# Kernel tuning notes

Hardware: AMD Instinct MI355X
Metric: run time of the kernel (lower is better)

The kernel has to match this reference:

```python
import jax, jax.numpy as jnp
import numpy as np

S, N, F = 32, 512, 256        # systems, atoms per system, feature/charge channels
R_EXCL = 5.0                  # neighbor_list_options.cutoff -> exclusion_radius
BOX = 30.0                    # box edge for random positions (Angstrom-scale)


def setup_inputs() -> dict:
    key = jax.random.key(0)
    k1, k2, k3, k4 = jax.random.split(key, 4)
    positions = jax.random.uniform(k1, (S, N, 3), dtype=jnp.float32) * BOX
    features = jax.random.normal(k2, (S * N, F), dtype=jnp.float32)
    W = jax.random.normal(k3, (F, F), dtype=jnp.float32) / jnp.sqrt(F)
    b = jax.random.normal(k4, (F,), dtype=jnp.float32) * 0.01
    return {"positions": positions, "features": features, "W": W, "b": b}


def _pair_potential(d):
    # CoulombPotential(smearing=None, exclusion_radius=R_EXCL).from_dist:
    # v(r) = (1/r) * (1 - f_cut(r)),  f_cut = 0.5*(1 + cos(pi*r/R_EXCL)) for r < R_EXCL
    fcut = jnp.where(d < R_EXCL, 0.5 * (1.0 + jnp.cos(jnp.pi * d / R_EXCL)), 0.0)
    return (1.0 / d) * (1.0 - fcut)


def reference(positions, features, W, b):
    # charges_map: Linear(F, F)
    charges = features @ W.T + b                      # [S*N, F]
    q = charges.reshape(S, N, F)                      # per-system charges

    # all-pairs distances per system (torch.combinations path, both directions
    # accumulated by the half-neighbor-list Calculator)
    diff = positions[:, :, None, :] - positions[:, None, :, :]   # [S,N,N,3]
    d = jnp.sqrt(jnp.sum(diff * diff, axis=-1))                  # [S,N,N]
    eye = jnp.eye(N, dtype=bool)
    d_safe = jnp.where(eye, 1.0, d)
    v = jnp.where(eye, 0.0, _pair_potential(d_safe))             # [S,N,N]

    # V_i = 0.5 * sum_j v(r_ij) q_j  (torchpme energy convention E = sum_i q_i V_i)
    V = 0.5 * jnp.einsum('sij,sjf->sif', v, q)                   # [S,N,F]

    # module returns potential * charges, concatenated over systems
    return (V * q).reshape(S * N, F)
```

## Files before the change

kernel.cpp:

```cpp
#include <hip/hip_runtime.h>
#include <hip/hip_cooperative_groups.h>

#define SY 32
#define NA 512
#define FD 256

typedef __attribute__((ext_vector_type(8))) short bf16x8;
typedef __attribute__((ext_vector_type(4))) short bf16x4;
typedef __attribute__((ext_vector_type(4))) float f32x4;

static __device__ __forceinline__ short f2bf(float x) {
    union { float f; unsigned u; } v; v.f = x;
    unsigned r = v.u + 0x7fffu + ((v.u >> 16) & 1u);
    return (short)(r >> 16);
}
static __device__ __forceinline__ float bf2f(short x) {
    union { float f; unsigned u; } v;
    v.u = ((unsigned)(unsigned short)x) << 16;
    return v.f;
}

__global__ __launch_bounds__(512) void charges_mfma(
    const float* __restrict__ feat, const float* __restrict__ W,
    const float* __restrict__ b, float* __restrict__ qfp,
    short* __restrict__ qT)
{
    __shared__ __attribute__((aligned(16))) short sA[64 * 72];
    __shared__ __attribute__((aligned(16))) short sB[256 * 72];
    __shared__ __attribute__((aligned(16))) short tr[256 * 72];
    const int t    = threadIdx.x;
    const int i0   = blockIdx.x * 64;
    const int w    = t >> 6;
    const int lane = t & 63;
    const int n16  = lane & 15;
    const int quad = lane >> 4;

    f32x4 acc[4][2];
    #pragma unroll
    for (int a = 0; a < 4; ++a)
        #pragma unroll
        for (int c = 0; c < 2; ++c) acc[a][c] = (f32x4)0.0f;

    for (int k0 = 0; k0 < FD; k0 += 64) {
        #pragma unroll
        for (int m = 0; m < 2; ++m) {
            int lin = t + 512 * m;
            int i = lin >> 4, kq = lin & 15;
            float4 v = *(const float4*)&feat[(size_t)(i0 + i) * FD + k0 + 4 * kq];
            bf16x4 p; p[0] = f2bf(v.x); p[1] = f2bf(v.y);
                      p[2] = f2bf(v.z); p[3] = f2bf(v.w);
            *(bf16x4*)&sA[i * 72 + 4 * kq] = p;
        }
        #pragma unroll
        for (int m = 0; m < 8; ++m) {
            int lin = t + 512 * m;
            int f = lin >> 4, kq = lin & 15;
            float4 v = *(const float4*)&W[(size_t)f * FD + k0 + 4 * kq];
            bf16x4 p; p[0] = f2bf(v.x); p[1] = f2bf(v.y);
                      p[2] = f2bf(v.z); p[3] = f2bf(v.w);
            *(bf16x4*)&sB[f * 72 + 4 * kq] = p;
        }
        __syncthreads();

        #pragma unroll
        for (int ks = 0; ks < 64; ks += 32) {
            bf16x8 af[4], bfr[2];
            #pragma unroll
            for (int it = 0; it < 4; ++it)
                af[it] = *(const bf16x8*)&sA[(16 * it + n16) * 72 + ks + quad * 8];
            #pragma unroll
            for (int fb = 0; fb < 2; ++fb)
                bfr[fb] = *(const bf16x8*)&sB[(32 * w + 16 * fb + n16) * 72 + ks + quad * 8];
            #pragma unroll
            for (int it = 0; it < 4; ++it)
                #pragma unroll
                for (int fb = 0; fb < 2; ++fb)
                    acc[it][fb] = __builtin_amdgcn_mfma_f32_16x16x32_bf16(
                        af[it], bfr[fb], acc[it][fb], 0, 0, 0);
        }
        __syncthreads();
    }

    float bias[2];
    #pragma unroll
    for (int fb = 0; fb < 2; ++fb) bias[fb] = b[32 * w + 16 * fb + n16];

    if (qfp) {
        #pragma unroll
        for (int it = 0; it < 4; ++it)
            #pragma unroll
            for (int fb = 0; fb < 2; ++fb)
                #pragma unroll
                for (int r = 0; r < 4; ++r) {
                    int i = i0 + 16 * it + 4 * quad + r;
                    int f = 32 * w + 16 * fb + n16;
                    qfp[(size_t)i * FD + f] = acc[it][fb][r] + bias[fb];
                }
    }

    #pragma unroll
    for (int it = 0; it < 4; ++it)
        #pragma unroll
        for (int fb = 0; fb < 2; ++fb) {
            bf16x4 p;
            #pragma unroll
            for (int r = 0; r < 4; ++r) p[r] = f2bf(acc[it][fb][r] + bias[fb]);
            int f = 32 * w + 16 * fb + n16;
            *(bf16x4*)&tr[f * 72 + 16 * it + 4 * quad] = p;
        }
    __syncthreads();
    {
        short* qTs = qT + ((size_t)(i0 >> 9)) * FD * NA;
        const int ilb = i0 & 511;
        #pragma unroll
        for (int n = 0; n < 4; ++n) {
            int S = n * 512 + t;
            int f = S >> 3;
            int c = S & 7;
            uint4 v = *(const uint4*)&tr[f * 72 + c * 8];
            *(uint4*)&qTs[(size_t)f * NA + ilb + c * 8] = v;
        }
    }
}

__global__ __launch_bounds__(256) void lr_fast(
    const float* __restrict__ pos, float* __restrict__ gbuf,
    const short* __restrict__ qT)
{
    __shared__ float px[NA], py[NA], pz[NA];
    __shared__ __attribute__((aligned(16))) short sqb[FD * 64];
    __shared__ __attribute__((aligned(16))) short svb[32 * 64];

    const int blk = blockIdx.x;
    const int s   = blk & 31;
    const int i0  = (blk >> 5) * 32;
    const int t   = threadIdx.x;
    const int w    = t >> 6;
    const int lane = t & 63;
    const int n16  = lane & 15;
    const int quad = lane >> 4;

    for (int m = t; m < NA; m += 256) {
        const float* p = &pos[((size_t)s * NA + m) * 3];
        px[m] = p[0]; py[m] = p[1]; pz[m] = p[2];
    }

    f32x4 acc[2][4];
    #pragma unroll
    for (int a = 0; a < 2; ++a)
        #pragma unroll
        for (int c = 0; c < 4; ++c) acc[a][c] = (f32x4)0.0f;
    float qreg[2][4][4];

    const short* qTs = qT + (size_t)s * FD * NA;
    const int pi = t & 31;
    const int pc = t >> 5;
    const int gi = i0 + pi;

    __syncthreads();
    const float xi = px[gi], yi = py[gi], zi = pz[gi];

    for (int j0 = 0; j0 < NA; j0 += 64) {
        #pragma unroll
        for (int n = 0; n < 8; ++n) {
            int S  = n * 256 + t;
            int f  = S >> 3;
            int cs = S & 7;
            int c  = (cs - f) & 7;
            uint4 v = *(const uint4*)&qTs[(size_t)f * NA + j0 + c * 8];
            *(uint4*)&sqb[f * 64 + cs * 8] = v;
        }
        bf16x8 vrow;
        #pragma unroll
        for (int jj = 0; jj < 8; ++jj) {
            int gj = j0 + pc * 8 + jj;
            float dx = xi - px[gj];
            float dy = yi - py[gj];
            float dz = zi - pz[gj];
            float r2 = dx * dx + dy * dy + dz * dz;
            float inv = __builtin_amdgcn_rsqf(r2);
            float dd  = r2 * inv;
            float sn = __sinf(dd * 0.31415926535f);
            float om = (dd < 5.0f) ? sn * sn : 1.0f;
            float vv = (gi != gj) ? 0.5f * om * inv : 0.0f;
            vrow[jj] = f2bf(vv);
        }
        *(bf16x8*)&svb[pi * 64 + (((pc + pi) & 7) * 8)] = vrow;
        __syncthreads();

        if (j0 == (i0 & ~63)) {
            const int jb0 = i0 & 63;
            #pragma unroll
            for (int it = 0; it < 2; ++it)
                #pragma unroll
                for (int fb = 0; fb < 4; ++fb) {
                    int f = 64 * w + 16 * fb + n16;
                    #pragma unroll
                    for (int r = 0; r < 4; ++r) {
                        int jl = jb0 + 16 * it + 4 * quad + r;
                        int c  = jl >> 3, o = jl & 7;
                        qreg[it][fb][r] =
                            bf2f(sqb[f * 64 + (((c + f) & 7) * 8) + o]);
                    }
                }
        }

        bf16x8 af[2][2], bfr[2][4];
        #pragma unroll
        for (int it = 0; it < 2; ++it)
            #pragma unroll
            for (int kh = 0; kh < 2; ++kh) {
                int i = 16 * it + n16;
                int c = kh * 4 + quad;
                af[it][kh] = *(const bf16x8*)&svb[i * 64 + (((c + i) & 7) * 8)];
            }
        #pragma unroll
        for (int fb = 0; fb < 4; ++fb)
            #pragma unroll
            for (int kh = 0; kh < 2; ++kh) {
                int f = 64 * w + 16 * fb + n16;
                int c = kh * 4 + quad;
                bfr[kh][fb] = *(const bf16x8*)&sqb[f * 64 + (((c + f) & 7) * 8)];
            }
        #pragma unroll
        for (int kh = 0; kh < 2; ++kh)
            #pragma unroll
            for (int it = 0; it < 2; ++it)
                #pragma unroll
                for (int fb = 0; fb < 4; ++fb)
                    acc[it][fb] = __builtin_amdgcn_mfma_f32_16x16x32_bf16(
                        af[it][kh], bfr[kh][fb], acc[it][fb], 0, 0, 0);
        __syncthreads();
    }

    #pragma unroll
    for (int it = 0; it < 2; ++it)
        #pragma unroll
        for (int fb = 0; fb < 4; ++fb)
            #pragma unroll
            for (int r = 0; r < 4; ++r) {
                int i = i0 + 16 * it + 4 * quad + r;
                int f = 64 * w + 16 * fb + n16;
                size_t a = ((size_t)s * NA + i) * FD + f;
                gbuf[a] = acc[it][fb][r] * qreg[it][fb][r];
            }
}

__global__ __launch_bounds__(256) void lr_coop(
    const float* __restrict__ pos, float* __restrict__ gbuf)
{
    __shared__ float px[NA], py[NA], pz[NA];
    __shared__ __attribute__((aligned(16))) short svb[64 * 40];
    __shared__ __attribute__((aligned(16))) short sqb[FD * 40];

    const int blk = blockIdx.x;
    const int s   = blk & 31;
    const int i0  = (blk >> 5) * 64;
    const int t   = threadIdx.x;
    const int w    = t >> 6;
    const int lane = t & 63;
    const int n16  = lane & 15;
    const int quad = lane >> 4;

    for (int m = t; m < NA; m += 256) {
        const float* p = &pos[((size_t)s * NA + m) * 3];
        px[m] = p[0]; py[m] = p[1]; pz[m] = p[2];
    }

    f32x4 acc[4][4];
    #pragma unroll
    for (int a = 0; a < 4; ++a)
        #pragma unroll
        for (int c = 0; c < 4; ++c) acc[a][c] = (f32x4)0.0f;

    __syncthreads();

    const int fq  = t >> 2;
    const int jb  = t & 3;
    const int iv  = t & 63;
    const int jbv = t >> 6;
    const int gi  = i0 + iv;

    float4 rq[8];
    #pragma unroll
    for (int m = 0; m < 8; ++m)
        rq[m] = *(const float4*)&gbuf[((size_t)s * NA + 8 * jb + m) * FD + 4 * fq];

    for (int j0 = 0; j0 < NA; j0 += 32) {
        bf16x8 vrow;
        #pragma unroll
        for (int jj = 0; jj < 8; ++jj) {
            int gj = j0 + 8 * jbv + jj;
            float dx = px[gi] - px[gj];
            float dy = py[gi] - py[gj];
            float dz = pz[gi] - pz[gj];
            float dd = sqrtf(dx * dx + dy * dy + dz * dz);
            float om = (dd < 5.0f) ? 0.5f * (1.0f - __cosf(dd * 0.62831853071795f))
                                   : 1.0f;
            float vv = (gi != gj) ? (0.5f * om * __builtin_amdgcn_rcpf(dd)) : 0.0f;
            vrow[jj] = f2bf(vv);
        }
        bf16x8 rows[4];
        #pragma unroll
        for (int m = 0; m < 8; ++m) {
            rows[0][m] = f2bf(rq[m].x);
            rows[1][m] = f2bf(rq[m].y);
            rows[2][m] = f2bf(rq[m].z);
            rows[3][m] = f2bf(rq[m].w);
        }
        #pragma unroll
        for (int d = 0; d < 4; ++d) {
            int f = 4 * fq + d;
            int phys = (jb + (f >> 3)) & 3;
            *(bf16x8*)&sqb[f * 40 + phys * 8] = rows[d];
        }
        {
            int phys = (jbv + (iv >> 3)) & 3;
            *(bf16x8*)&svb[iv * 40 + phys * 8] = vrow;
        }
        {
            int jn = (j0 + 32) & (NA - 1);
            #pragma unroll
            for (int m = 0; m < 8; ++m)
                rq[m] = *(const float4*)&gbuf[((size_t)s * NA + jn + 8 * jb + m) * FD + 4 * fq];
        }
        __syncthreads();

        bf16x8 af[4], bfr[4];
        #pragma unroll
        for (int it = 0; it < 4; ++it) {
            int i = 16 * it + n16;
            int phys = (quad + (i >> 3)) & 3;
            af[it] = *(const bf16x8*)&svb[i * 40 + phys * 8];
        }
        #pragma unroll
        for (int fb = 0; fb < 4; ++fb) {
            int f = 16 * (4 * w + fb) + n16;
            int phys = (quad + (f >> 3)) & 3;
            bfr[fb] = *(const bf16x8*)&sqb[f * 40 + phys * 8];
        }
        #pragma unroll
        for (int it = 0; it < 4; ++it)
            #pragma unroll
            for (int fb = 0; fb < 4; ++fb)
                acc[it][fb] = __builtin_amdgcn_mfma_f32_16x16x32_bf16(
                    af[it], bfr[fb], acc[it][fb], 0, 0, 0);
        __syncthreads();
    }

    cooperative_groups::this_grid().sync();

    #pragma unroll
    for (int it = 0; it < 4; ++it)
        #pragma unroll
        for (int fb = 0; fb < 4; ++fb)
            #pragma unroll
            for (int r = 0; r < 4; ++r) {
                int i = i0 + 16 * it + 4 * quad + r;
                int f = 16 * (4 * w + fb) + n16;
                size_t a = ((size_t)s * NA + i) * FD + f;
                gbuf[a] = acc[it][fb][r] * gbuf[a];
            }
}

extern "C" void kernel_launch(void* const* d_in, const int* in_sizes, int n_in,
                              void* d_out, int out_size, void* d_ws, size_t ws_size,
                              hipStream_t stream) {
    const float* positions = (const float*)d_in[0];
    const float* features  = (const float*)d_in[1];
    const float* W         = (const float*)d_in[2];
    const float* b         = (const float*)d_in[3];
    float* gbuf = (float*)d_out;

    const size_t qT_bytes = (size_t)SY * NA * FD * sizeof(short);
    const bool fast = (ws_size >= qT_bytes);
    short* qT = fast ? (short*)d_ws : nullptr;

    if (fast) {
        charges_mfma<<<dim3(256), 512, 0, stream>>>(features, W, b, nullptr, qT);
        lr_fast<<<dim3(512), 256, 0, stream>>>(positions, gbuf, qT);
    } else {
        charges_mfma<<<dim3(256), 512, 0, stream>>>(features, W, b, gbuf,
                                                    (short*)d_out );
        void* args[] = {(void*)&positions, (void*)&gbuf};
        hipLaunchCooperativeKernel((void*)lr_coop, dim3(256), dim3(256),
                                   args, 0, stream);
    }
}
```

Baseline: 110.2 us.

## Pre-convert W to bf16, retile charges GEMM, split lr_fast over features with prefetch

A new prep_w kernel converts W to bf16 once per call, so the charges GEMM loads bf16 W directly instead of converting the whole W in every block. The charges kernel now uses 32-row tiles on 256 threads, giving 512 blocks, and reuses sB as the transpose buffer. lr_fast splits the feature dimension into two halves, giving 1024 blocks with a smaller LDS footprint and launch_bounds(256,4) to raise occupancy. It also register-prefetches the next q tile while computing the pair potential. The costs are an extra launch, recomputing the pair potentials twice per system tile, and higher register pressure from the prefetch.

After: 125.8 us. 1.14x slower.

```diff
diff --git a/kernel.cpp b/kernel.cpp
--- a/kernel.cpp
+++ b/kernel.cpp
@@ -20,120 +20,141 @@
     return v.f;
 }
 
-__global__ __launch_bounds__(512) void charges_mfma(
-    const float* __restrict__ feat, const float* __restrict__ W,
-    const float* __restrict__ b, float* __restrict__ qfp,
-    short* __restrict__ qT)
+__global__ __launch_bounds__(256) void prep_w(
+    const float* __restrict__ W, short* __restrict__ Wb)
 {
-    __shared__ __attribute__((aligned(16))) short sA[64 * 72];
+    int idx = (blockIdx.x * 256 + threadIdx.x) * 4;
+    float4 v = *(const float4*)&W[idx];
+    bf16x4 p; p[0] = f2bf(v.x); p[1] = f2bf(v.y);
+              p[2] = f2bf(v.z); p[3] = f2bf(v.w);
+    *(bf16x4*)&Wb[idx] = p;
+}
+
+__global__ __launch_bounds__(256) void charges_v3(
+    const float* __restrict__ feat, const float* __restrict__ Wfp,
+    const short* __restrict__ Wb, const float* __restrict__ b,
+    float* __restrict__ qfp, short* __restrict__ qT)
+{
+    __shared__ __attribute__((aligned(16))) short sA[32 * 72];
     __shared__ __attribute__((aligned(16))) short sB[256 * 72];
-    __shared__ __attribute__((aligned(16))) short tr[256 * 72];
     const int t    = threadIdx.x;
-    const int i0   = blockIdx.x * 64;
+    const int i0   = blockIdx.x * 32;
     const int w    = t >> 6;
     const int lane = t & 63;
     const int n16  = lane & 15;
     const int quad = lane >> 4;
 
-    f32x4 acc[4][2];
-    #pragma unroll
-    for (int a = 0; a < 4; ++a)
-        #pragma unroll
-        for (int c = 0; c < 2; ++c) acc[a][c] = (f32x4)0.0f;
+    f32x4 acc[2][4];
+    #pragma unroll
+    for (int a = 0; a < 2; ++a)
+        #pragma unroll
+        for (int c = 0; c < 4; ++c) acc[a][c] = (f32x4)0.0f;
 
     for (int k0 = 0; k0 < FD; k0 += 64) {
         #pragma unroll
         for (int m = 0; m < 2; ++m) {
-            int lin = t + 512 * m;
-            int i = lin >> 4, kq = lin & 15;
-            float4 v = *(const float4*)&feat[(size_t)(i0 + i) * FD + k0 + 4 * kq];
+            int lin = t + 256 * m;
+            int row = lin >> 4, kq = lin & 15;
+            float4 v = *(const float4*)&feat[(size_t)(i0 + row) * FD + k0 + 4 * kq];
             bf16x4 p; p[0] = f2bf(v.x); p[1] = f2bf(v.y);
                       p[2] = f2bf(v.z); p[3] = f2bf(v.w);
-            *(bf16x4*)&sA[i * 72 + 4 * kq] = p;
-        }
-        #pragma unroll
-        for (int m = 0; m < 8; ++m) {
-            int lin = t + 512 * m;
-            int f = lin >> 4, kq = lin & 15;
-            float4 v = *(const float4*)&W[(size_t)f * FD + k0 + 4 * kq];
-            bf16x4 p; p[0] = f2bf(v.x); p[1] = f2bf(v.y);
-                      p[2] = f2bf(v.z); p[3] = f2bf(v.w);
-            *(bf16x4*)&sB[f * 72 + 4 * kq] = p;
+            *(bf16x4*)&sA[row * 72 + 4 * kq] = p;
+        }
+        if (Wb) {
+            #pragma unroll
+            for (int n = 0; n < 8; ++n) {
+                int S = t + 256 * n;
+                int f = S >> 3, c = S & 7;
+                uint4 v = *(const uint4*)&Wb[(size_t)f * FD + k0 + c * 8];
+                *(uint4*)&sB[f * 72 + c * 8] = v;
+            }
+        } else {
+            #pragma unroll
+            for (int m = 0; m < 16; ++m) {
+                int lin = t + 256 * m;
+                int f = lin >> 4, kq = lin & 15;
+                float4 v = *(const float4*)&Wfp[(size_t)f * FD + k0 + 4 * kq];
+                bf16x4 p; p[0] = f2bf(v.x); p[1] = f2bf(v.y);
+                          p[2] = f2bf(v.z); p[3] = f2bf(v.w);
+                *(bf16x4*)&sB[f * 72 + 4 * kq] = p;
+            }
         }
         __syncthreads();
 
         #pragma unroll
         for (int ks = 0; ks < 64; ks += 32) {
-            bf16x8 af[4], bfr[2];
-            #pragma unroll
-            for (int it = 0; it < 4; ++it)
+            bf16x8 af[2], bfr[4];
+            #pragma unroll
+            for (int it = 0; it < 2; ++it)
                 af[it] = *(const bf16x8*)&sA[(16 * it + n16) * 72 + ks + quad * 8];
             #pragma unroll
-            for (int fb = 0; fb < 2; ++fb)
-                bfr[fb] = *(const bf16x8*)&sB[(32 * w + 16 * fb + n16) * 72 + ks + quad * 8];
-            #pragma unroll
-            for (int it = 0; it < 4; ++it)
+            for (int fb = 0; fb < 4; ++fb)
+                bfr[fb] = *(const bf16x8*)&sB[(64 * w + 16 * fb + n16) * 72 + ks + quad * 8];
+            #pragma unroll
+            for (int it = 0; it < 2; ++it)
                 #pragma unroll
-                for (int fb = 0; fb < 2; ++fb)
+                for (int fb = 0; fb < 4; ++fb)
                     acc[it][fb] = __builtin_amdgcn_mfma_f32_16x16x32_bf16(
                         af[it], bfr[fb], acc[it][fb], 0, 0, 0);
         }
         __syncthreads();
     }
 
-    float bias[2];
-    #pragma unroll
-    for (int fb = 0; fb < 2; ++fb) bias[fb] = b[32 * w + 16 * fb + n16];
+    float bias[4];
+    #pragma unroll
+    for (int fb = 0; fb < 4; ++fb) bias[fb] = b[64 * w + 16 * fb + n16];
 
     if (qfp) {
         #pragma unroll
-        for (int it = 0; it < 4; ++it)
-            #pragma unroll
-            for (int fb = 0; fb < 2; ++fb)
+        for (int it = 0; it < 2; ++it)
+            #pragma unroll
+            for (int fb = 0; fb < 4; ++fb)
                 #pragma unroll
                 for (int r = 0; r < 4; ++r) {
                     int i = i0 + 16 * it + 4 * quad + r;
-                    int f = 32 * w + 16 * fb + n16;
+                    int f = 64 * w + 16 * fb + n16;
                     qfp[(size_t)i * FD + f] = acc[it][fb][r] + bias[fb];
                 }
     }
 
-    #pragma unroll
-    for (int it = 0; it < 4; ++it)
-        #pragma unroll
-        for (int fb = 0; fb < 2; ++fb) {
-            bf16x4 p;
-            #pragma unroll
-            for (int r = 0; r < 4; ++r) p[r] = f2bf(acc[it][fb][r] + bias[fb]);
-            int f = 32 * w + 16 * fb + n16;
-            *(bf16x4*)&tr[f * 72 + 16 * it + 4 * quad] = p;
-        }
-    __syncthreads();
-    {
+    if (qT) {
+        short* tr = sB;
+        #pragma unroll
+        for (int it = 0; it < 2; ++it)
+            #pragma unroll
+            for (int fb = 0; fb < 4; ++fb) {
+                bf16x4 p;
+                #pragma unroll
+                for (int r = 0; r < 4; ++r) p[r] = f2bf(acc[it][fb][r] + bias[fb]);
+                int f = 64 * w + 16 * fb + n16;
+                *(bf16x4*)&tr[f * 40 + 16 * it + 4 * quad] = p;
+            }
+        __syncthreads();
         short* qTs = qT + ((size_t)(i0 >> 9)) * FD * NA;
         const int ilb = i0 & 511;
         #pragma unroll
         for (int n = 0; n < 4; ++n) {
-            int S = n * 512 + t;
-            int f = S >> 3;
-            int c = S & 7;
-            uint4 v = *(const uint4*)&tr[f * 72 + c * 8];
+            int S = t + 256 * n;
+            int f = S >> 2, c = S & 3;
+            uint4 v = *(const uint4*)&tr[f * 40 + c * 8];
             *(uint4*)&qTs[(size_t)f * NA + ilb + c * 8] = v;
         }
     }
 }
 
-__global__ __launch_bounds__(256) void lr_fast(
-    const float* __restrict__ pos, float* __restrict__ gbuf,
+__global__ __launch_bounds__(256, 4) void lr_fast(
+    const float* __restrict__ pos, float* __restrict__ out,
     const short* __restrict__ qT)
 {
     __shared__ float px[NA], py[NA], pz[NA];
-    __shared__ __attribute__((aligned(16))) short sqb[FD * 64];
+    __shared__ __attribute__((aligned(16))) short sqb[128 * 64];
     __shared__ __attribute__((aligned(16))) short svb[32 * 64];
 
     const int blk = blockIdx.x;
     const int s   = blk & 31;
-    const int i0  = (blk >> 5) * 32;
+    const int rr  = blk >> 5;
+    const int i0  = (rr & 15) * 32;
+    const int f0  = (rr >> 4) * 128;
     const int t   = threadIdx.x;
     const int w    = t >> 6;
     const int lane = t & 63;
@@ -145,30 +166,39 @@
         px[m] = p[0]; py[m] = p[1]; pz[m] = p[2];
     }
 
-    f32x4 acc[2][4];
+    f32x4 acc[2][2];
     #pragma unroll
     for (int a = 0; a < 2; ++a)
         #pragma unroll
-        for (int c = 0; c < 4; ++c) acc[a][c] = (f32x4)0.0f;
-    float qreg[2][4][4];
-
-    const short* qTs = qT + (size_t)s * FD * NA;
+        for (int c = 0; c < 2; ++c) acc[a][c] = (f32x4)0.0f;
+    float qreg[2][2][4];
+
+    const short* qTs = qT + (size_t)s * FD * NA + (size_t)f0 * NA;
     const int pi = t & 31;
     const int pc = t >> 5;
     const int gi = i0 + pi;
 
+    const int sfl[1] = {};  (void)sfl;
+    uint4 pf[4];
+    #pragma unroll
+    for (int n = 0; n < 4; ++n) {
+        int S  = t + 256 * n;
+        int fl = S >> 3;
+        int cs = S & 7;
+        int c  = (cs - fl) & 7;
+        pf[n] = *(const uint4*)&qTs[(size_t)fl * NA + 0 + c * 8];
+    }
+
     __syncthreads();
     const float xi = px[gi], yi = py[gi], zi = pz[gi];
 
     for (int j0 = 0; j0 < NA; j0 += 64) {
         #pragma unroll
-        for (int n = 0; n < 8; ++n) {
-            int S  = n * 256 + t;
-            int f  = S >> 3;
+        for (int n = 0; n < 4; ++n) {
+            int S  = t + 256 * n;
+            int fl = S >> 3;
             int cs = S & 7;
-            int c  = (cs - f) & 7;
-            uint4 v = *(const uint4*)&qTs[(size_t)f * NA + j0 + c * 8];
-            *(uint4*)&sqb[f * 64 + cs * 8] = v;
+            *(uint4*)&sqb[fl * 64 + cs * 8] = pf[n];
         }
         bf16x8 vrow;
         #pragma unroll
@@ -186,6 +216,17 @@
             vrow[jj] = f2bf(vv);
         }
         *(bf16x8*)&svb[pi * 64 + (((pc + pi) & 7) * 8)] = vrow;
+        {
+            int jn = (j0 + 64) & (NA - 1);
+            #pragma unroll
+            for (int n = 0; n < 4; ++n) {
+                int S  = t + 256 * n;
+                int fl = S >> 3;
+                int cs = S & 7;
+                int c  = (cs - fl) & 7;
+                pf[n] = *(const uint4*)&qTs[(size_t)fl * NA + jn + c * 8];
+            }
+        }
         __syncthreads();
 
         if (j0 == (i0 & ~63)) {
@@ -193,19 +234,19 @@
             #pragma unroll
             for (int it = 0; it < 2; ++it)
                 #pragma unroll
-                for (int fb = 0; fb < 4; ++fb) {
-                    int f = 64 * w + 16 * fb + n16;
+                for (int fb = 0; fb < 2; ++fb) {
+                    int fl = 32 * w + 16 * fb + n16;
                     #pragma unroll
                     for (int r = 0; r < 4; ++r) {
                         int jl = jb0 + 16 * it + 4 * quad + r;
                         int c  = jl >> 3, o = jl & 7;
                         qreg[it][fb][r] =
-                            bf2f(sqb[f * 64 + (((c + f) & 7) * 8) + o]);
+                            bf2f(sqb[fl * 64 + (((c + fl) & 7) * 8) + o]);
                     }
                 }
         }
 
-        bf16x8 af[2][2], bfr[2][4];
+        bf16x8 af[2][2], bfr[2][2];
         #pragma unroll
         for (int it = 0; it < 2; ++it)
             #pragma unroll
@@ -215,19 +256,19 @@
                 af[it][kh] = *(const bf16x8*)&svb[i * 64 + (((c + i) & 7) * 8)];
             }
         #pragma unroll
-        for (int fb = 0; fb < 4; ++fb)
+        for (int fb = 0; fb < 2; ++fb)
             #pragma unroll
             for (int kh = 0; kh < 2; ++kh) {
-                int f = 64 * w + 16 * fb + n16;
-                int c = kh * 4 + quad;
-                bfr[kh][fb] = *(const bf16x8*)&sqb[f * 64 + (((c + f) & 7) * 8)];
+                int fl = 32 * w + 16 * fb + n16;
+                int c  = kh * 4 + quad;
+                bfr[kh][fb] = *(const bf16x8*)&sqb[fl * 64 + (((c + fl) & 7) * 8)];
             }
         #pragma unroll
         for (int kh = 0; kh < 2; ++kh)
             #pragma unroll
             for (int it = 0; it < 2; ++it)
                 #pragma unroll
-                for (int fb = 0; fb < 4; ++fb)
+                for (int fb = 0; fb < 2; ++fb)
                     acc[it][fb] = __builtin_amdgcn_mfma_f32_16x16x32_bf16(
                         af[it][kh], bfr[kh][fb], acc[it][fb], 0, 0, 0);
         __syncthreads();
@@ -236,13 +277,13 @@
     #pragma unroll
     for (int it = 0; it < 2; ++it)
         #pragma unroll
-        for (int fb = 0; fb < 4; ++fb)
+        for (int fb = 0; fb < 2; ++fb)
             #pragma unroll
             for (int r = 0; r < 4; ++r) {
                 int i = i0 + 16 * it + 4 * quad + r;
-                int f = 64 * w + 16 * fb + n16;
+                int f = f0 + 32 * w + 16 * fb + n16;
                 size_t a = ((size_t)s * NA + i) * FD + f;
-                gbuf[a] = acc[it][fb][r] * qreg[it][fb][r];
+                out[a] = acc[it][fb][r] * qreg[it][fb][r];
             }
 }
 
@@ -372,16 +413,18 @@
     const float* b         = (const float*)d_in[3];
     float* gbuf = (float*)d_out;
 
-    const size_t qT_bytes = (size_t)SY * NA * FD * sizeof(short);
-    const bool fast = (ws_size >= qT_bytes);
-    short* qT = fast ? (short*)d_ws : nullptr;
+    const size_t qT_elems = (size_t)SY * NA * FD;
+    const size_t need = (qT_elems + FD * FD) * sizeof(short);
+    const bool fast = (ws_size >= need);
 
     if (fast) {
-        charges_mfma<<<dim3(256), 512, 0, stream>>>(features, W, b, nullptr, qT);
-        lr_fast<<<dim3(512), 256, 0, stream>>>(positions, gbuf, qT);
+        short* qT = (short*)d_ws;
+        short* Wb = (short*)d_ws + qT_elems;
+        prep_w<<<dim3(64), 256, 0, stream>>>(W, Wb);
+        charges_v3<<<dim3(512), 256, 0, stream>>>(features, W, Wb, b, nullptr, qT);
+        lr_fast<<<dim3(1024), 256, 0, stream>>>(positions, gbuf, qT);
     } else {
-        charges_mfma<<<dim3(256), 512, 0, stream>>>(features, W, b, gbuf,
-                                                    (short*)d_out );
+        charges_v3<<<dim3(512), 256, 0, stream>>>(features, W, nullptr, b, gbuf, nullptr);
         void* args[] = {(void*)&positions, (void*)&gbuf};
         hipLaunchCooperativeKernel((void*)lr_coop, dim3(256), dim3(256),
                                    args, 0, stream);
```
